# Performance work log

Hardware: AMD Instinct MI355X
Metric: run time of the kernel (lower is better)

Reference implementation:

```python
import jax, jax.numpy as jnp
import numpy as np

LAMBD = 1.0  # margin, matches init kwarg lambd
N, C, D = 16384, 4096, 128


def setup_inputs() -> dict:
    key = jax.random.key(0)
    k1, k2, k3 = jax.random.split(key, 3)
    embeddings = jax.random.normal(k1, (N, D), dtype=jnp.float32)
    targets = jax.random.randint(k2, (N,), 0, C, dtype=jnp.int64)
    centers = jax.random.normal(k3, (C, D), dtype=jnp.float32)
    return {"embeddings": embeddings, "targets": targets, "centers": centers}


def reference(embeddings, targets, centers):
    # Squared euclidean distances from every sample to every center, [n, C],
    # via ||e||^2 + ||c||^2 - 2 e.c (avoids the [n, C, d] broadcast tensor).
    e2 = jnp.sum(embeddings * embeddings, axis=-1, keepdims=True)          # [n, 1]
    c2 = jnp.sum(centers * centers, axis=-1)                               # [C]
    dist = e2 + c2[None, :] - 2.0 * jnp.matmul(embeddings, centers.T)      # [n, C]

    tgt = targets.astype(jnp.int32)
    ap = jnp.take_along_axis(dist, tgt[:, None], axis=1)                   # [n, 1]

    # loss_val[i, c] = lambd + d(e_i, center_{y_i}) - d(e_i, center_c)
    loss_val = LAMBD + ap - dist                                           # [n, C]

    # Triplet (i, y_i, c) is mined iff loss_val > 0 and c != y_i.
    not_label = jnp.arange(dist.shape[1], dtype=jnp.int32)[None, :] != tgt[:, None]
    mask = (loss_val > 0.0) & not_label

    # For mined triplets relu(ap - an + lambd) == loss_val (already > 0).
    total = jnp.sum(jnp.where(mask, loss_val, 0.0))
    cnt = jnp.sum(mask).astype(loss_val.dtype)
    # If no triplet violates the margin, the original returns 0.
    return jnp.where(cnt > 0.0, total / jnp.maximum(cnt, 1.0), 0.0)
```

## Files before the change

### kernel.cpp

```cpp
#include <hip/hip_runtime.h>

#define N_SAMP 16384
#define N_CENT 4096
#define DIM    128
#define LAMBD  1.0f
#define NSLOT  256

typedef _Float16 half4v __attribute__((ext_vector_type(4)));
typedef _Float16 half8  __attribute__((ext_vector_type(8)));
typedef float    floatx4 __attribute__((ext_vector_type(4)));

struct Slot { float sum; unsigned int cnt; unsigned int pad[30]; };

__device__ __forceinline__ void gload_lds16(const void* g, void* l) {
  __builtin_amdgcn_global_load_lds(
      (__attribute__((address_space(1))) void*)(g),
      (__attribute__((address_space(3))) void*)(l), 16, 0, 0);
}

__global__ __launch_bounds__(256) void prep_kernel(
    const float* __restrict__ E, const float* __restrict__ Cc,
    const int* __restrict__ tgt,
    _Float16* __restrict__ Eh, _Float16* __restrict__ Ch,
    float* __restrict__ c2, float* __restrict__ rowk,
    Slot* __restrict__ slots) {
  const int tid  = threadIdx.x;
  const int w    = tid >> 6;
  const int lane = tid & 63;
  const int l    = lane & 31;
  const int E_BLOCKS = N_SAMP / 8;

  if ((int)blockIdx.x < E_BLOCKS) {
    if (blockIdx.x == 0) {
      slots[tid].sum = 0.f; slots[tid].cnt = 0u; slots[tid].pad[0] = 0u;
    }
    const int wv = blockIdx.x * 4 + w;
    const int r0 = wv * 2 + (lane >> 5);
    float4 e = *(const float4*)(E + (size_t)r0 * DIM + l * 4);
    const int yi = tgt[r0];
    float4 c = *(const float4*)(Cc + (size_t)yi * DIM + l * 4);
    float s = c.x * (c.x - 2.f * e.x) + c.y * (c.y - 2.f * e.y)
            + c.z * (c.z - 2.f * e.z) + c.w * (c.w - 2.f * e.w);
    #pragma unroll
    for (int off = 16; off > 0; off >>= 1) s += __shfl_xor(s, off);
    if (l == 0) rowk[r0] = LAMBD + s;
    half4v h;
    h[0] = (_Float16)(2.f * e.x); h[1] = (_Float16)(2.f * e.y);
    h[2] = (_Float16)(2.f * e.z); h[3] = (_Float16)(2.f * e.w);
    *(half4v*)(Eh + (size_t)r0 * DIM + l * 4) = h;
  } else {
    const int wv = ((int)blockIdx.x - E_BLOCKS) * 4 + w;
    const int r0 = wv * 2 + (lane >> 5);
    float4 c = *(const float4*)(Cc + (size_t)r0 * DIM + l * 4);
    float s = c.x * c.x + c.y * c.y + c.z * c.z + c.w * c.w;
    #pragma unroll
    for (int off = 16; off > 0; off >>= 1) s += __shfl_xor(s, off);
    if (l == 0) c2[r0] = s;
    half4v h;
    h[0] = (_Float16)c.x; h[1] = (_Float16)c.y;
    h[2] = (_Float16)c.z; h[3] = (_Float16)c.w;
    *(half4v*)(Ch + (size_t)r0 * DIM + l * 4) = h;
  }
}

__global__ __launch_bounds__(512, 2) void center_gemm_kernel(
    const _Float16* __restrict__ Eh, const _Float16* __restrict__ Ch,
    const float* __restrict__ c2, const float* __restrict__ rowk,
    Slot* __restrict__ slots, float* __restrict__ out) {
  __shared__ _Float16 As[2][128 * DIM];
  __shared__ _Float16 Bs[256 * DIM];
  __shared__ float swsum[8];
  __shared__ unsigned int swcnt[8];
  __shared__ int tktS;

  const int tid  = threadIdx.x;
  const int w    = tid >> 6;
  const int lane = tid & 63;

  const int bid    = blockIdx.x;
  const int xcd    = bid & 7;
  const int j      = bid >> 3;
  const int bm_grp = xcd * 2 + (j & 1);
  const int bn_grp = j >> 1;
  const int bn0    = bn_grp * 256;

  const int p  = lane & 15;
  const int r4 = lane >> 4;

  {
    const char* gB = (const char*)(Ch + (size_t)bn0 * DIM);
    char* lB = (char*)Bs;
    #pragma unroll
    for (int it = 0; it < 8; ++it) {
      const int chunk = w * 8 + it;
      const int row   = chunk * 4 + r4;
      gload_lds16(gB + row * 256 + (p ^ (row & 15)) * 16, lB + chunk * 1024);
    }
    const char* gA = (const char*)(Eh + (size_t)bm_grp * 8 * 128 * DIM);
    char* lA = (char*)As[0];
    #pragma unroll
    for (int it = 0; it < 4; ++it) {
      const int chunk = w * 4 + it;
      const int row   = chunk * 4 + r4;
      gload_lds16(gA + row * 256 + (p ^ (row & 15)) * 16, lA + chunk * 1024);
    }
  }

  const int wm = w >> 2, wn = w & 3;
  const int q = lane >> 4, r = lane & 15;
  const int row0 = wm * 64, col0 = wn * 64;

  float c2v[4];
  #pragma unroll
  for (int nt = 0; nt < 4; ++nt) c2v[nt] = c2[bn0 + col0 + nt * 16 + r];

  const float* rkbase = rowk + bm_grp * 8 * 128;
  floatx4 rkc[4], rkn[4];
  #pragma unroll
  for (int mt = 0; mt < 4; ++mt)
    rkc[mt] = *(const floatx4*)(rkbase + row0 + mt * 16 + q * 4);

  __syncthreads();

  half8 bf[4][4];
  #pragma unroll
  for (int nt = 0; nt < 4; ++nt)
    #pragma unroll
    for (int ks = 0; ks < 4; ++ks)
      bf[nt][ks] = *(const half8*)&Bs[(col0 + nt * 16 + r) * DIM + (((ks * 4 + q) ^ r) * 8)];

  float lsum = 0.f;
  unsigned int cntU = 0u;

  for (int t = 0; t < 8; ++t) {
    const int cur = t & 1;

    if (t < 7) {
      const char* gA = (const char*)(Eh + (size_t)(bm_grp * 8 + t + 1) * 128 * DIM);
      char* lA = (char*)As[cur ^ 1];
      #pragma unroll
      for (int it = 0; it < 4; ++it) {
        const int chunk = w * 4 + it;
        const int row   = chunk * 4 + r4;
        gload_lds16(gA + row * 256 + (p ^ (row & 15)) * 16, lA + chunk * 1024);
      }
      #pragma unroll
      for (int mt = 0; mt < 4; ++mt)
        rkn[mt] = *(const floatx4*)(rkbase + (t + 1) * 128 + row0 + mt * 16 + q * 4);
    }

    floatx4 acc[4][4];
    #pragma unroll
    for (int mt = 0; mt < 4; ++mt)
      #pragma unroll
      for (int nt = 0; nt < 4; ++nt)
        acc[mt][nt] = rkc[mt] - c2v[nt];

    #pragma unroll
    for (int ks = 0; ks < 4; ++ks) {
      const int cidx = ks * 4 + q;
      half8 af[4];
      #pragma unroll
      for (int mt = 0; mt < 4; ++mt)
        af[mt] = *(const half8*)&As[cur][(row0 + mt * 16 + r) * DIM + ((cidx ^ r) * 8)];
      #pragma unroll
      for (int mt = 0; mt < 4; ++mt)
        #pragma unroll
        for (int nt = 0; nt < 4; ++nt)
          acc[mt][nt] = __builtin_amdgcn_mfma_f32_16x16x32_f16(af[mt], bf[nt][ks], acc[mt][nt], 0, 0, 0);
    }

    #pragma unroll
    for (int mt = 0; mt < 4; ++mt)
      #pragma unroll
      for (int nt = 0; nt < 4; ++nt) {
        const floatx4 a = acc[mt][nt];
        #pragma unroll
        for (int rg = 0; rg < 4; ++rg) {
          const float v = a[rg];
          lsum += fmaxf(v, 0.f);
          cntU += (unsigned int)__popcll(__ballot(v > 0.f));
        }
      }

    __syncthreads();
    #pragma unroll
    for (int mt = 0; mt < 4; ++mt) rkc[mt] = rkn[mt];
  }

  #pragma unroll
  for (int off = 32; off > 0; off >>= 1) lsum += __shfl_down(lsum, off);
  if (lane == 0) { swsum[w] = lsum; swcnt[w] = cntU; }
  __syncthreads();
  if (tid == 0) {
    float s = 0.f; unsigned int c = 0u;
    #pragma unroll
    for (int k = 0; k < 8; ++k) { s += swsum[k]; c += swcnt[k]; }
    Slot* sl = &slots[bid];
    atomicAdd(&sl->sum, s);
    atomicAdd(&sl->cnt, c);
    __threadfence();
    tktS = (int)atomicAdd(&slots[0].pad[0], 1u);
  }
  __syncthreads();

  if (tktS == NSLOT - 1) {
    float s = 0.f; unsigned int c = 0u;
    if (tid < NSLOT) {
      s = atomicAdd(&slots[tid].sum, 0.f);
      c = atomicAdd(&slots[tid].cnt, 0u);
    }
    #pragma unroll
    for (int off = 32; off > 0; off >>= 1) {
      s += __shfl_down(s, off);
      c += __shfl_down(c, off);
    }
    if (lane == 0) { swsum[w] = s; swcnt[w] = c; }
    __syncthreads();
    if (tid == 0) {
      float S = 0.f; unsigned int C = 0u;
      #pragma unroll
      for (int k = 0; k < 8; ++k) { S += swsum[k]; C += swcnt[k]; }
      const float Sc = S - (float)N_SAMP * LAMBD;
      const long long Cc2 = (long long)C - (long long)N_SAMP;
      out[0] = (Cc2 > 0) ? (Sc / (float)Cc2) : 0.f;
    }
  }
}

__global__ void zero_kernel(float* ws_sum, unsigned int* ws_cnt) {
  if (threadIdx.x == 0) { *ws_sum = 0.f; *ws_cnt = 0u; }
}

__global__ void finalize_simple(const float* __restrict__ ws_sum,
                                const unsigned int* __restrict__ ws_cnt,
                                float* __restrict__ out) {
  if (threadIdx.x == 0 && blockIdx.x == 0) {
    const unsigned int c = *ws_cnt;
    out[0] = (c > 0u) ? (*ws_sum / (float)c) : 0.f;
  }
}

__global__ __launch_bounds__(256) void fallback_kernel(
    const float* __restrict__ E, const float* __restrict__ Cc,
    const int* __restrict__ tgt,
    float* __restrict__ ws_sum, unsigned int* __restrict__ ws_cnt) {
  __shared__ float eS[DIM];
  __shared__ float apS;
  const int i = blockIdx.x;
  const int tid = threadIdx.x;
  if (tid < DIM) eS[tid] = E[(size_t)i * DIM + tid];
  __syncthreads();
  const int yi = tgt[i];
  float dloc[16];
  #pragma unroll
  for (int j = 0; j < 16; ++j) {
    const int c = tid + 256 * j;
    const float* cp = Cc + (size_t)c * DIM;
    float s = 0.f;
    for (int d = 0; d < DIM; d += 4) {
      float4 cv = *(const float4*)(cp + d);
      s += cv.x * (cv.x - 2.f * eS[d + 0]) + cv.y * (cv.y - 2.f * eS[d + 1])
         + cv.z * (cv.z - 2.f * eS[d + 2]) + cv.w * (cv.w - 2.f * eS[d + 3]);
    }
    dloc[j] = s;
    if (c == yi) apS = s;
  }
  __syncthreads();
  const float apv = apS;
  float lsum = 0.f; int lcnt = 0;
  #pragma unroll
  for (int j = 0; j < 16; ++j) {
    const int c = tid + 256 * j;
    const float v = LAMBD + apv - dloc[j];
    const bool mined = (v > 0.f) & (c != yi);
    lsum += mined ? v : 0.f;
    lcnt += mined ? 1 : 0;
  }
  #pragma unroll
  for (int off = 32; off > 0; off >>= 1) {
    lsum += __shfl_down(lsum, off);
    lcnt += __shfl_down(lcnt, off);
  }
  __shared__ float swsum[4];
  __shared__ int   swcnt[4];
  const int w = tid >> 6, lane = tid & 63;
  if (lane == 0) { swsum[w] = lsum; swcnt[w] = lcnt; }
  __syncthreads();
  if (tid == 0) {
    atomicAdd(ws_sum, swsum[0] + swsum[1] + swsum[2] + swsum[3]);
    atomicAdd(ws_cnt, (unsigned int)(swcnt[0] + swcnt[1] + swcnt[2] + swcnt[3]));
  }
}

extern "C" void kernel_launch(void* const* d_in, const int* in_sizes, int n_in,
                              void* d_out, int out_size, void* d_ws, size_t ws_size,
                              hipStream_t stream) {
  const float* E   = (const float*)d_in[0];
  const int*   tgt = (const int*)d_in[1];
  const float* Cc  = (const float*)d_in[2];
  float* out = (float*)d_out;

  const size_t EH_BYTES = (size_t)N_SAMP * DIM * 2;
  const size_t CH_BYTES = (size_t)N_CENT * DIM * 2;
  const size_t C2_BYTES = (size_t)N_CENT * 4;
  const size_t RK_BYTES = (size_t)N_SAMP * 4;
  const size_t SL_BYTES = (size_t)NSLOT * sizeof(Slot);
  const size_t NEEDED = EH_BYTES + CH_BYTES + C2_BYTES + RK_BYTES + SL_BYTES;

  char* ws = (char*)d_ws;
  if (ws_size >= NEEDED) {
    _Float16* Eh = (_Float16*)ws;
    _Float16* Ch = (_Float16*)(ws + EH_BYTES);
    float* c2    = (float*)(ws + EH_BYTES + CH_BYTES);
    float* rowk  = (float*)(ws + EH_BYTES + CH_BYTES + C2_BYTES);
    Slot* slots  = (Slot*)(ws + EH_BYTES + CH_BYTES + C2_BYTES + RK_BYTES);

    const int E_BLOCKS = N_SAMP / 8;
    const int C_BLOCKS = N_CENT / 8;
    prep_kernel<<<E_BLOCKS + C_BLOCKS, 256, 0, stream>>>(
        E, Cc, tgt, Eh, Ch, c2, rowk, slots);
    center_gemm_kernel<<<256, 512, 0, stream>>>(Eh, Ch, c2, rowk, slots, out);
  } else {
    float* ws_sum = (float*)ws;
    unsigned int* ws_cnt = (unsigned int*)(ws_sum + 1);
    zero_kernel<<<1, 64, 0, stream>>>(ws_sum, ws_cnt);
    fallback_kernel<<<N_SAMP, 256, 0, stream>>>(E, Cc, tgt, ws_sum, ws_cnt);
    finalize_simple<<<1, 64, 0, stream>>>(ws_sum, ws_cnt, out);
  }
}
```

Baseline: 96.43 us.

## Fuse prep and GEMM into one cooperative kernel with grid sync

Merges the fp16 conversion and norm prep pass into the GEMM kernel using a cooperative launch and a grid-wide barrier, removing a separate kernel launch. The prep work is spread over 256 blocks of 512 threads instead of 2560 small blocks. The per-slot reduction is replaced by a single global atomic accumulator with a ticket counter. This risks lower parallelism during the prep phase, grid-sync overhead, and contention on a single atomic location. It falls back to the old two-kernel path if cooperative launch is unavailable.

```diff
diff --git a/kernel.cpp b/kernel.cpp
--- a/kernel.cpp
+++ b/kernel.cpp
@@ -1,4 +1,7 @@
 #include <hip/hip_runtime.h>
+#include <hip/hip_cooperative_groups.h>
+
+namespace cg = cooperative_groups;
 
 #define N_SAMP 16384
 #define N_CENT 4096
@@ -10,12 +13,200 @@
 typedef _Float16 half8  __attribute__((ext_vector_type(8)));
 typedef float    floatx4 __attribute__((ext_vector_type(4)));
 
+struct Red { float sum; unsigned int cnt; unsigned int tkt; unsigned int pad[29]; };
 struct Slot { float sum; unsigned int cnt; unsigned int pad[30]; };
 
 __device__ __forceinline__ void gload_lds16(const void* g, void* l) {
   __builtin_amdgcn_global_load_lds(
       (__attribute__((address_space(1))) void*)(g),
       (__attribute__((address_space(3))) void*)(l), 16, 0, 0);
+}
+
+__global__ __launch_bounds__(512, 2) void fused_kernel(
+    const float* __restrict__ E, const float* __restrict__ Cc,
+    const int* __restrict__ tgt,
+    _Float16* __restrict__ Eh, _Float16* __restrict__ Ch,
+    float* __restrict__ c2, float* __restrict__ rowk,
+    Red* __restrict__ red, float* __restrict__ out) {
+  __shared__ _Float16 As[2][128 * DIM];
+  __shared__ _Float16 Bs[256 * DIM];
+  __shared__ float swsum[8];
+  __shared__ unsigned int swcnt[8];
+
+  const int tid  = threadIdx.x;
+  const int bid  = blockIdx.x;
+  const int w    = tid >> 6;
+  const int lane = tid & 63;
+
+  {
+    const int h = tid >> 5;
+    const int l = tid & 31;
+    if (bid == 0 && tid == 0) { red->sum = 0.f; red->cnt = 0u; red->tkt = 0u; }
+    const int erow0 = (bid & 7) * 2048 + (bid >> 3) * 64;
+    #pragma unroll
+    for (int it = 0; it < 4; ++it) {
+      const int row = erow0 + it * 16 + h;
+      float4 e = *(const float4*)(E + (size_t)row * DIM + l * 4);
+      const int yi = tgt[row];
+      float4 c = *(const float4*)(Cc + (size_t)yi * DIM + l * 4);
+      float s = c.x * (c.x - 2.f * e.x) + c.y * (c.y - 2.f * e.y)
+              + c.z * (c.z - 2.f * e.z) + c.w * (c.w - 2.f * e.w);
+      #pragma unroll
+      for (int off = 16; off > 0; off >>= 1) s += __shfl_xor(s, off);
+      if (l == 0) rowk[row] = LAMBD + s;
+      half4v hv;
+      hv[0] = (_Float16)(2.f * e.x); hv[1] = (_Float16)(2.f * e.y);
+      hv[2] = (_Float16)(2.f * e.z); hv[3] = (_Float16)(2.f * e.w);
+      *(half4v*)(Eh + (size_t)row * DIM + l * 4) = hv;
+    }
+    {
+      const int row = bid * 16 + h;
+      float4 c = *(const float4*)(Cc + (size_t)row * DIM + l * 4);
+      float s = c.x * c.x + c.y * c.y + c.z * c.z + c.w * c.w;
+      #pragma unroll
+      for (int off = 16; off > 0; off >>= 1) s += __shfl_xor(s, off);
+      if (l == 0) c2[row] = s;
+      half4v hv;
+      hv[0] = (_Float16)c.x; hv[1] = (_Float16)c.y;
+      hv[2] = (_Float16)c.z; hv[3] = (_Float16)c.w;
+      *(half4v*)(Ch + (size_t)row * DIM + l * 4) = hv;
+    }
+  }
+  __threadfence();
+  cg::this_grid().sync();
+  __threadfence();
+
+  const int xcd    = bid & 7;
+  const int j      = bid >> 3;
+  const int bm_grp = xcd * 2 + (j & 1);
+  const int bn_grp = j >> 1;
+  const int bn0    = bn_grp * 256;
+
+  const int p  = lane & 15;
+  const int r4 = lane >> 4;
+
+  {
+    const char* gB = (const char*)(Ch + (size_t)bn0 * DIM);
+    char* lB = (char*)Bs;
+    #pragma unroll
+    for (int it = 0; it < 8; ++it) {
+      const int chunk = w * 8 + it;
+      const int row   = chunk * 4 + r4;
+      gload_lds16(gB + row * 256 + (p ^ (row & 15)) * 16, lB + chunk * 1024);
+    }
+    const char* gA = (const char*)(Eh + (size_t)bm_grp * 8 * 128 * DIM);
+    char* lA = (char*)As[0];
+    #pragma unroll
+    for (int it = 0; it < 4; ++it) {
+      const int chunk = w * 4 + it;
+      const int row   = chunk * 4 + r4;
+      gload_lds16(gA + row * 256 + (p ^ (row & 15)) * 16, lA + chunk * 1024);
+    }
+  }
+
+  const int wm = w >> 2, wn = w & 3;
+  const int q = lane >> 4, r = lane & 15;
+  const int row0 = wm * 64, col0 = wn * 64;
+
+  float c2v[4];
+  #pragma unroll
+  for (int nt = 0; nt < 4; ++nt) c2v[nt] = c2[bn0 + col0 + nt * 16 + r];
+
+  const float* rkbase = rowk + bm_grp * 8 * 128;
+  floatx4 rkc[4], rkn[4];
+  #pragma unroll
+  for (int mt = 0; mt < 4; ++mt)
+    rkc[mt] = *(const floatx4*)(rkbase + row0 + mt * 16 + q * 4);
+
+  __syncthreads();
+
+  half8 bf[4][4];
+  #pragma unroll
+  for (int nt = 0; nt < 4; ++nt)
+    #pragma unroll
+    for (int ks = 0; ks < 4; ++ks)
+      bf[nt][ks] = *(const half8*)&Bs[(col0 + nt * 16 + r) * DIM + (((ks * 4 + q) ^ r) * 8)];
+
+  float lsum = 0.f;
+  unsigned int cntU = 0u;
+
+  for (int t = 0; t < 8; ++t) {
+    const int cur = t & 1;
+
+    if (t < 7) {
+      const char* gA = (const char*)(Eh + (size_t)(bm_grp * 8 + t + 1) * 128 * DIM);
+      char* lA = (char*)As[cur ^ 1];
+      #pragma unroll
+      for (int it = 0; it < 4; ++it) {
+        const int chunk = w * 4 + it;
+        const int row   = chunk * 4 + r4;
+        gload_lds16(gA + row * 256 + (p ^ (row & 15)) * 16, lA + chunk * 1024);
+      }
+      #pragma unroll
+      for (int mt = 0; mt < 4; ++mt)
+        rkn[mt] = *(const floatx4*)(rkbase + (t + 1) * 128 + row0 + mt * 16 + q * 4);
+    }
+
+    floatx4 acc[4][4];
+    #pragma unroll
+    for (int mt = 0; mt < 4; ++mt)
+      #pragma unroll
+      for (int nt = 0; nt < 4; ++nt)
+        acc[mt][nt] = rkc[mt] - c2v[nt];
+
+    #pragma unroll
+    for (int ks = 0; ks < 4; ++ks) {
+      const int cidx = ks * 4 + q;
+      half8 af[4];
+      #pragma unroll
+      for (int mt = 0; mt < 4; ++mt)
+        af[mt] = *(const half8*)&As[cur][(row0 + mt * 16 + r) * DIM + ((cidx ^ r) * 8)];
+      #pragma unroll
+      for (int mt = 0; mt < 4; ++mt)
+        #pragma unroll
+        for (int nt = 0; nt < 4; ++nt)
+          acc[mt][nt] = __builtin_amdgcn_mfma_f32_16x16x32_f16(af[mt], bf[nt][ks], acc[mt][nt], 0, 0, 0);
+    }
+
+    #pragma unroll
+    for (int mt = 0; mt < 4; ++mt)
+      #pragma unroll
+      for (int nt = 0; nt < 4; ++nt) {
+        const floatx4 a = acc[mt][nt];
+        #pragma unroll
+        for (int rg = 0; rg < 4; ++rg) {
+          const float v = a[rg];
+          lsum += fmaxf(v, 0.f);
+          cntU += (unsigned int)__popcll(__ballot(v > 0.f));
+        }
+      }
+
+    __syncthreads();
+    #pragma unroll
+    for (int mt = 0; mt < 4; ++mt) rkc[mt] = rkn[mt];
+  }
+
+  #pragma unroll
+  for (int off = 32; off > 0; off >>= 1) lsum += __shfl_down(lsum, off);
+  if (lane == 0) { swsum[w] = lsum; swcnt[w] = cntU; }
+  __syncthreads();
+  if (tid == 0) {
+    float s = 0.f; unsigned int c = 0u;
+    #pragma unroll
+    for (int k = 0; k < 8; ++k) { s += swsum[k]; c += swcnt[k]; }
+    atomicAdd(&red->sum, s);
+    atomicAdd(&red->cnt, c);
+    __threadfence();
+    const unsigned int t = atomicAdd(&red->tkt, 1u);
+    if (t == NSLOT - 1) {
+      __threadfence();
+      const float S = atomicAdd(&red->sum, 0.f);
+      const unsigned int C = atomicAdd(&red->cnt, 0u);
+      const float Sc = S - (float)N_SAMP * LAMBD;
+      const long long Cn = (long long)C - (long long)N_SAMP;
+      out[0] = (Cn > 0) ? (Sc / (float)Cn) : 0.f;
+    }
+  }
 }
 
 __global__ __launch_bounds__(256) void prep_kernel(
@@ -134,7 +325,6 @@
 
   for (int t = 0; t < 8; ++t) {
     const int cur = t & 1;
-
     if (t < 7) {
       const char* gA = (const char*)(Eh + (size_t)(bm_grp * 8 + t + 1) * 128 * DIM);
       char* lA = (char*)As[cur ^ 1];
@@ -222,8 +412,8 @@
       #pragma unroll
       for (int k = 0; k < 8; ++k) { S += swsum[k]; C += swcnt[k]; }
       const float Sc = S - (float)N_SAMP * LAMBD;
-      const long long Cc2 = (long long)C - (long long)N_SAMP;
-      out[0] = (Cc2 > 0) ? (Sc / (float)Cc2) : 0.f;
+      const long long Cn = (long long)C - (long long)N_SAMP;
+      out[0] = (Cn > 0) ? (Sc / (float)Cn) : 0.f;
     }
   }
 }
@@ -308,14 +498,33 @@
   const size_t SL_BYTES = (size_t)NSLOT * sizeof(Slot);
   const size_t NEEDED = EH_BYTES + CH_BYTES + C2_BYTES + RK_BYTES + SL_BYTES;
 
+  static int coop_ok = -1;
+  if (coop_ok < 0) {
+    int dev = 0, v = 0;
+    hipGetDevice(&dev);
+    hipDeviceGetAttribute(&v, hipDeviceAttributeCooperativeLaunch, dev);
+    coop_ok = v;
+  }
+
   char* ws = (char*)d_ws;
   if (ws_size >= NEEDED) {
     _Float16* Eh = (_Float16*)ws;
     _Float16* Ch = (_Float16*)(ws + EH_BYTES);
     float* c2    = (float*)(ws + EH_BYTES + CH_BYTES);
     float* rowk  = (float*)(ws + EH_BYTES + CH_BYTES + C2_BYTES);
-    Slot* slots  = (Slot*)(ws + EH_BYTES + CH_BYTES + C2_BYTES + RK_BYTES);
-
+    char* slbase = ws + EH_BYTES + CH_BYTES + C2_BYTES + RK_BYTES;
+
+    if (coop_ok) {
+      Red* red = (Red*)slbase;
+      void* args[] = {(void*)&E, (void*)&Cc, (void*)&tgt, (void*)&Eh,
+                      (void*)&Ch, (void*)&c2, (void*)&rowk, (void*)&red,
+                      (void*)&out};
+      hipError_t err = hipLaunchCooperativeKernel(
+          (const void*)fused_kernel, dim3(256), dim3(512), args, 0, stream);
+      if (err == hipSuccess) return;
+      coop_ok = 0;
+    }
+    Slot* slots = (Slot*)slbase;
     const int E_BLOCKS = N_SAMP / 8;
     const int C_BLOCKS = N_CENT / 8;
     prep_kernel<<<E_BLOCKS + C_BLOCKS, 256, 0, stream>>>(
```

Result: slower. 203.7 us (+111.3%).
